# Kernel tuning notes

Hardware: AMD Instinct MI355X
Metric: run time of the kernel (lower is better)

The kernel has to match this reference:

```python
import jax, jax.numpy as jnp
import numpy as np

TOP_K = 2
LN_EPS = 1e-5
GATE_EPS = 1e-6


def setup_inputs() -> dict:
    key = jax.random.key(0)
    ks = jax.random.split(key, 5)
    B, D, E, H, O = 16384, 1200, 8, 1024, 1
    x = jax.random.normal(ks[0], (B, D), dtype=jnp.float32)
    w_gate = jax.random.normal(ks[1], (D, E), dtype=jnp.float32) * 0.05
    W1 = jax.random.normal(ks[2], (E, D, H), dtype=jnp.float32) * (1.0 / np.sqrt(D))
    b1 = jnp.zeros((E, H), dtype=jnp.float32)
    g1 = jnp.ones((E, H), dtype=jnp.float32)   # LayerNorm weight
    be1 = jnp.zeros((E, H), dtype=jnp.float32)  # LayerNorm bias
    W2 = jax.random.normal(ks[3], (E, H, O), dtype=jnp.float32) * (1.0 / np.sqrt(H))
    b2 = jnp.zeros((E, O), dtype=jnp.float32)
    return {"x": x, "w_gate": w_gate, "W1": W1, "b1": b1, "g1": g1, "be1": be1, "W2": W2, "b2": b2}


def reference(x, w_gate, W1, b1, g1, be1, W2, b2):
    B = x.shape[0]
    # --- top-k gating (eval mode: no noise) ---
    probs = jax.nn.softmax(x @ w_gate, axis=1)                 # [B, E]
    top_vals, top_idx = jax.lax.top_k(probs, TOP_K)            # [B, k]
    top_gates = top_vals / (jnp.sum(top_vals, axis=1, keepdims=True) + GATE_EPS)
    gates = jnp.zeros_like(probs).at[jnp.arange(B)[:, None], top_idx].set(top_gates)  # [B, E]
    # --- per-expert MLP (computed densely for all experts; gates zero out non-selected) ---
    h = jnp.einsum('bd,edh->beh', x, W1) + b1                  # [B, E, H]
    mu = jnp.mean(h, axis=-1, keepdims=True)
    var = jnp.var(h, axis=-1, keepdims=True)
    h = (h - mu) * jax.lax.rsqrt(var + LN_EPS) * g1 + be1      # LayerNorm
    h = jax.nn.relu(h)
    out = jax.nn.sigmoid(jnp.einsum('beh,eho->beo', h, W2) + b2)  # [B, E, O]
    # --- scatter/combine: weighted sum over experts ---
    y = jnp.einsum('be,beo->bo', gates, out)                   # [B, O]
    return y
```

## Files before the change

kernel.cpp:

```cpp
#include <hip/hip_runtime.h>
#include <hip/hip_bf16.h>
#include <stdint.h>

#define B_ROWS 16384
#define D_IN   1200
#define D_PAD  1216
#define N_EXP  8
#define H_DIM  1024
#define R_CAP  4608
#define CAP    36864
#define N_RT   288
#define LN_EPS 1e-5f
#define GATE_EPS 1e-6f
#define CNT_STRIDE 16

#define O_CNT    0
#define O_PROWC  512
#define O_PGATEC 147968
#define O_XBF    295424
#define O_W1T    40143744
#define O_HBUF   60066688

#define GATING_BLOCKS (B_ROWS / 16)
#define W1T_BLOCKS    (19 * 16 * 8)
#define PREP_BLOCKS   (GATING_BLOCKS + 1 + W1T_BLOCKS)

#define NT        (D_PAD / 32)
#define SLOT_SZ   16384

typedef short bf16x8 __attribute__((ext_vector_type(8)));
typedef short short8 __attribute__((ext_vector_type(8)));
typedef short short4v __attribute__((ext_vector_type(4)));
typedef float f32x4 __attribute__((ext_vector_type(4)));

__device__ __forceinline__ void load_lds16(const void* gptr, void* ldsptr) {
    __builtin_amdgcn_global_load_lds(
        (__attribute__((address_space(1))) void*)const_cast<void*>(gptr),
        (__attribute__((address_space(3))) void*)ldsptr, 16, 0, 0);
}

__device__ __forceinline__ short4v pack_bf16x4(float4 a) {
    union { short4v v; __hip_bfloat16 h[4]; } u;
    u.h[0] = __float2bfloat16(a.x); u.h[1] = __float2bfloat16(a.y);
    u.h[2] = __float2bfloat16(a.z); u.h[3] = __float2bfloat16(a.w);
    return u.v;
}

__global__ __launch_bounds__(256) void prep_kernel(
    const float* __restrict__ x, const float* __restrict__ wg,
    int* __restrict__ cnt, int* __restrict__ pairRowC, float* __restrict__ pairGateC,
    __hip_bfloat16* __restrict__ xbf, float* __restrict__ y,
    const float* __restrict__ W1, __hip_bfloat16* __restrict__ w1t)
{
    __shared__ int lcnt[N_EXP];
    __shared__ int base[N_EXP];
    __shared__ float tile[2][32][33];
    int bx = blockIdx.x;
    int tid = threadIdx.x;

    if (bx > GATING_BLOCKS) {
        int b = bx - GATING_BLOCKS - 1;
        int d0 = (b % 19) * 64;
        int h0 = ((b / 19) % 16) * 64;
        int e = b / (19 * 16);
        const float* src = W1 + (long)e * D_IN * H_DIM;

        int hs = tid & 15;
        int dr = tid >> 4;
#pragma unroll
        for (int s = 0; s < 4; ++s) {
            int dl = dr + 16 * s;
            int d = d0 + dl;
            float4 v = (d < D_IN)
                ? ((const float4*)(src + (long)d * H_DIM + h0))[hs]
                : (float4){0.f, 0.f, 0.f, 0.f};
            int drl = dl & 31;
            int hl = hs * 4;
            int Th = hl >> 5;
            int hh = hl & 31;
            tile[Th][drl][hh + 0] = v.x;
            tile[Th][drl][hh + 1] = v.y;
            tile[Th][drl][hh + 2] = v.z;
            tile[Th][drl][hh + 3] = v.w;
            if (s == 1) {
                __syncthreads();
                int T2 = tid >> 7, rr = tid & 127;
                int hl2 = rr >> 2, dseg = rr & 3;
                float f[8];
#pragma unroll
                for (int jj = 0; jj < 8; ++jj) f[jj] = tile[T2][dseg * 8 + jj][hl2];
                union { short8 v8; __hip_bfloat16 hh8[8]; } u;
#pragma unroll
                for (int jj = 0; jj < 8; ++jj) u.hh8[jj] = __float2bfloat16(f[jj]);
                int h = h0 + T2 * 32 + hl2;
                ((short8*)(w1t + (long)e * H_DIM * D_PAD + (long)h * D_PAD + d0))[dseg] = u.v8;
                __syncthreads();
            }
        }
        __syncthreads();
        {
            int T2 = tid >> 7, rr = tid & 127;
            int hl2 = rr >> 2, dseg = rr & 3;
            float f[8];
#pragma unroll
            for (int jj = 0; jj < 8; ++jj) f[jj] = tile[T2][dseg * 8 + jj][hl2];
            union { short8 v8; __hip_bfloat16 hh8[8]; } u;
#pragma unroll
            for (int jj = 0; jj < 8; ++jj) u.hh8[jj] = __float2bfloat16(f[jj]);
            int h = h0 + T2 * 32 + hl2;
            ((short8*)(w1t + (long)e * H_DIM * D_PAD + (long)h * D_PAD + d0 + 32))[dseg] = u.v8;
        }
        return;
    }

    if (bx == GATING_BLOCKS) {
        short8* xrow = (short8*)(xbf + (long)B_ROWS * D_PAD);
        if (tid < 152) xrow[tid] = (short8){0, 0, 0, 0, 0, 0, 0, 0};
        return;
    }

    if (tid < N_EXP) lcnt[tid] = 0;
    if (tid < 16) y[bx * 16 + tid] = 0.f;
    __syncthreads();

    int widx = tid >> 6;
    int lane = tid & 63;
    int rowbase = bx * 16 + widx * 4;
    const float* xw = x + (long)rowbase * D_IN;

    float acc[4][8];
#pragma unroll
    for (int r = 0; r < 4; ++r)
#pragma unroll
        for (int e = 0; e < N_EXP; ++e) acc[r][e] = 0.f;

    for (int i = lane; i < 304; i += 64) {
        if (i < 300) {
            const float4* wv4 = (const float4*)(wg + (long)i * 32);
            float4 w0 = wv4[0], w1v = wv4[1], w2 = wv4[2], w3 = wv4[3],
                   w4 = wv4[4], w5 = wv4[5], w6 = wv4[6], w7 = wv4[7];
#pragma unroll
            for (int r = 0; r < 4; ++r) {
                float4 xv = ((const float4*)(xw + (long)r * D_IN))[i];
                acc[r][0] += xv.x * w0.x + xv.y * w2.x + xv.z * w4.x + xv.w * w6.x;
                acc[r][1] += xv.x * w0.y + xv.y * w2.y + xv.z * w4.y + xv.w * w6.y;
                acc[r][2] += xv.x * w0.z + xv.y * w2.z + xv.z * w4.z + xv.w * w6.z;
                acc[r][3] += xv.x * w0.w + xv.y * w2.w + xv.z * w4.w + xv.w * w6.w;
                acc[r][4] += xv.x * w1v.x + xv.y * w3.x + xv.z * w5.x + xv.w * w7.x;
                acc[r][5] += xv.x * w1v.y + xv.y * w3.y + xv.z * w5.y + xv.w * w7.y;
                acc[r][6] += xv.x * w1v.z + xv.y * w3.z + xv.z * w5.z + xv.w * w7.z;
                acc[r][7] += xv.x * w1v.w + xv.y * w3.w + xv.z * w5.w + xv.w * w7.w;
                ((short4v*)(xbf + (long)(rowbase + r) * D_PAD))[i] = pack_bf16x4(xv);
            }
        } else {
#pragma unroll
            for (int r = 0; r < 4; ++r)
                ((short4v*)(xbf + (long)(rowbase + r) * D_PAD))[i] = (short4v){0, 0, 0, 0};
        }
    }

#pragma unroll
    for (int r = 0; r < 4; ++r)
#pragma unroll
        for (int e = 0; e < N_EXP; ++e) {
            float v = acc[r][e];
#pragma unroll
            for (int off = 32; off > 0; off >>= 1) v += __shfl_xor(v, off, 64);
            acc[r][e] = v;
        }

    float my[N_EXP];
#pragma unroll
    for (int e = 0; e < N_EXP; ++e) my[e] = acc[0][e];
#pragma unroll
    for (int r = 1; r < 4; ++r)
#pragma unroll
        for (int e = 0; e < N_EXP; ++e)
            if (lane == r) my[e] = acc[r][e];

    int i0 = 0, i1 = 1, s0 = 0, s1 = 0;
    float g0 = 0.f, g1 = 0.f;
    if (lane < 4) {
        float m = my[0];
#pragma unroll
        for (int e = 1; e < N_EXP; ++e) m = fmaxf(m, my[e]);
        float p[N_EXP], s = 0.f;
#pragma unroll
        for (int e = 0; e < N_EXP; ++e) { p[e] = expf(my[e] - m); s += p[e]; }
#pragma unroll
        for (int e = 1; e < N_EXP; ++e) if (p[e] > p[i0]) i0 = e;
        i1 = (i0 == 0) ? 1 : 0;
#pragma unroll
        for (int e = 0; e < N_EXP; ++e) if (e != i0 && p[e] > p[i1]) i1 = e;
        float v0 = p[i0] / s, v1 = p[i1] / s;
        float inv = 1.f / (v0 + v1 + GATE_EPS);
        g0 = v0 * inv; g1 = v1 * inv;
        s0 = atomicAdd(&lcnt[i0], 1);
        s1 = atomicAdd(&lcnt[i1], 1);
    }
    __syncthreads();
    if (tid < N_EXP) base[tid] = atomicAdd(&cnt[tid * CNT_STRIDE], lcnt[tid]);
    __syncthreads();
    if (lane < 4) {
        int row = rowbase + lane;
        int p0 = i0 * R_CAP + base[i0] + s0;
        pairRowC[p0] = row; pairGateC[p0] = g0;
        int p1 = i1 * R_CAP + base[i1] + s1;
        pairRowC[p1] = row; pairGateC[p1] = g1;
    }
}

__global__ __launch_bounds__(256) void gemm_kernel(
    const __hip_bfloat16* __restrict__ xbf, const __hip_bfloat16* __restrict__ w1t,
    const float* __restrict__ b1, const int* __restrict__ cnt,
    const int* __restrict__ pairRowC,
    __hip_bfloat16* __restrict__ hbuf)
{
    int bi = blockIdx.x;
    int xcd = bi & 7;
    int j = bi >> 3;
    int col0 = (j & 7) << 7;
    int rt = xcd * 36 + (j >> 3);
    int row0 = rt << 7;
    int e = xcd;
    int cnt_e = cnt[e * CNT_STRIDE];
    if (row0 - e * R_CAP >= cnt_e) return;

    __shared__ __attribute__((aligned(128))) char lds[3 * SLOT_SZ];

    int t = threadIdx.x;
    int lane = t & 63, w = t >> 6;
    int wm = (w >> 1) * 64, wn = (w & 1) * 64;
    int l15 = lane & 15, quad = lane >> 4;
    int qsw = quad ^ ((l15 >> 1) & 3);

    f32x4 acc[4][4];
#pragma unroll
    for (int i = 0; i < 4; ++i)
#pragma unroll
        for (int j2 = 0; j2 < 4; ++j2) acc[i][j2] = (f32x4){0.f, 0.f, 0.f, 0.f};

    int r1 = t >> 2, seg = t & 3;
    int sw = seg ^ ((r1 >> 1) & 3);
    int ridx1 = pairRowC[row0 + r1];
    int ridx2 = pairRowC[row0 + 64 + r1];
    ridx1 = ((unsigned)ridx1 > B_ROWS) ? B_ROWS : ridx1;
    ridx2 = ((unsigned)ridx2 > B_ROWS) ? B_ROWS : ridx2;
    const __hip_bfloat16* Arow1 = xbf + (long)ridx1 * D_PAD + sw * 8;
    const __hip_bfloat16* Arow2 = xbf + (long)ridx2 * D_PAD + sw * 8;
    const __hip_bfloat16* Bb = w1t + (long)e * H_DIM * D_PAD + (long)col0 * D_PAD;
    const __hip_bfloat16* Brow1 = Bb + (long)r1 * D_PAD + sw * 8;
    const __hip_bfloat16* Brow2 = Bb + (long)(r1 + 64) * D_PAD + sw * 8;

#define STAGE(sl, koff) do { \
    char* sb_ = lds + (sl) * SLOT_SZ; \
    load_lds16(Arow1 + (koff), sb_ + t * 16); \
    load_lds16(Arow2 + (koff), sb_ + 4096 + t * 16); \
    load_lds16(Brow1 + (koff), sb_ + 8192 + t * 16); \
    load_lds16(Brow2 + (koff), sb_ + 12288 + t * 16); } while (0)

    STAGE(0, 0);
    STAGE(1, 32);
    asm volatile("s_waitcnt vmcnt(4)" ::: "memory");
    __builtin_amdgcn_s_barrier();
    asm volatile("" ::: "memory");

    int cur = 0;
    for (int kt = 0; kt < NT; ++kt) {
        int nxt2 = cur + 2; if (nxt2 >= 3) nxt2 -= 3;
        if (kt + 2 < NT) STAGE(nxt2, (kt + 2) * 32);

        const char* lAc = lds + cur * SLOT_SZ;
        const char* lBc = lAc + 8192;
        bf16x8 af[4], bfr[4];
#pragma unroll
        for (int i = 0; i < 4; ++i)
            af[i] = *(const bf16x8*)(lAc + (wm + i * 16 + l15) * 64 + qsw * 16);
#pragma unroll
        for (int j2 = 0; j2 < 4; ++j2)
            bfr[j2] = *(const bf16x8*)(lBc + (wn + j2 * 16 + l15) * 64 + qsw * 16);
#pragma unroll
        for (int i = 0; i < 4; ++i)
#pragma unroll
            for (int j2 = 0; j2 < 4; ++j2)
                acc[i][j2] = __builtin_amdgcn_mfma_f32_16x16x32_bf16(af[i], bfr[j2], acc[i][j2], 0, 0, 0);

        if (kt + 2 < NT)      asm volatile("s_waitcnt vmcnt(4)" ::: "memory");
        else if (kt + 1 < NT) asm volatile("s_waitcnt vmcnt(0)" ::: "memory");
        if (kt + 1 < NT) {
            __builtin_amdgcn_s_barrier();
            asm volatile("" ::: "memory");
        }
        cur += 1; if (cur >= 3) cur -= 3;
    }
#undef STAGE

#pragma unroll
    for (int i = 0; i < 4; ++i) {
        int lr = wm + i * 16 + quad * 4;
#pragma unroll
        for (int j2 = 0; j2 < 4; ++j2) {
            int gc = col0 + wn + j2 * 16 + l15;
            float bias = b1[e * H_DIM + gc];
#pragma unroll
            for (int r = 0; r < 4; ++r) {
                float v = acc[i][j2][r] + bias;
                hbuf[(long)(row0 + lr + r) * H_DIM + gc] = __float2bfloat16(v);
            }
        }
    }
}

__global__ __launch_bounds__(256) void ln_head_kernel(
    const __hip_bfloat16* __restrict__ hbuf, const int* __restrict__ cnt,
    const int* __restrict__ pairRowC, const float* __restrict__ pairGateC,
    const float* __restrict__ g1, const float* __restrict__ be1,
    const float* __restrict__ W2, const float* __restrict__ b2,
    float* __restrict__ y)
{
    int tid = threadIdx.x;
    int p = blockIdx.x * 4 + (tid >> 6);
    int e = p / R_CAP;
    int slot = p - e * R_CAP;
    if (slot >= cnt[e * CNT_STRIDE]) return;

    int lane = tid & 63;
    int row = pairRowC[p];
    float gate = pairGateC[p];
    const short4v* hr = (const short4v*)(hbuf + (long)p * H_DIM);

    float v[16];
    float sum = 0.f, sumsq = 0.f;
#pragma unroll
    for (int k = 0; k < 4; ++k) {
        union { short4v s; __hip_bfloat16 h[4]; } hv;
        hv.s = hr[lane + k * 64];
#pragma unroll
        for (int j = 0; j < 4; ++j) {
            float f = __bfloat162float(hv.h[j]);
            v[k * 4 + j] = f;
            sum += f;
            sumsq += f * f;
        }
    }
#pragma unroll
    for (int off = 32; off > 0; off >>= 1) {
        sum += __shfl_xor(sum, off, 64);
        sumsq += __shfl_xor(sumsq, off, 64);
    }
    float mu = sum * (1.f / H_DIM);
    float var = sumsq * (1.f / H_DIM) - mu * mu;
    float rstd = rsqrtf(var + LN_EPS);

    float z = 0.f;
#pragma unroll
    for (int k = 0; k < 4; ++k) {
        float4 gv = ((const float4*)(g1 + e * H_DIM))[lane + k * 64];
        float4 bv = ((const float4*)(be1 + e * H_DIM))[lane + k * 64];
        float4 wv = ((const float4*)(W2 + e * H_DIM))[lane + k * 64];
        z += fmaxf((v[k*4+0] - mu) * rstd * gv.x + bv.x, 0.f) * wv.x;
        z += fmaxf((v[k*4+1] - mu) * rstd * gv.y + bv.y, 0.f) * wv.y;
        z += fmaxf((v[k*4+2] - mu) * rstd * gv.z + bv.z, 0.f) * wv.z;
        z += fmaxf((v[k*4+3] - mu) * rstd * gv.w + bv.w, 0.f) * wv.w;
    }
#pragma unroll
    for (int off = 32; off > 0; off >>= 1) z += __shfl_xor(z, off, 64);
    if (lane == 0) {
        float zt = z + b2[e];
        float o = 1.f / (1.f + expf(-zt));
        atomicAdd(&y[row], gate * o);
    }
}

extern "C" void kernel_launch(void* const* d_in, const int* in_sizes, int n_in,
                              void* d_out, int out_size, void* d_ws, size_t ws_size,
                              hipStream_t stream)
{
    const float* x   = (const float*)d_in[0];
    const float* wg  = (const float*)d_in[1];
    const float* W1  = (const float*)d_in[2];
    const float* b1  = (const float*)d_in[3];
    const float* g1  = (const float*)d_in[4];
    const float* be1 = (const float*)d_in[5];
    const float* W2  = (const float*)d_in[6];
    const float* b2  = (const float*)d_in[7];
    float* y = (float*)d_out;

    char* ws = (char*)d_ws;
    int*   cnt       = (int*)(ws + O_CNT);
    int*   pairRowC  = (int*)(ws + O_PROWC);
    float* pairGateC = (float*)(ws + O_PGATEC);
    __hip_bfloat16* xbf  = (__hip_bfloat16*)(ws + O_XBF);
    __hip_bfloat16* w1t  = (__hip_bfloat16*)(ws + O_W1T);
    __hip_bfloat16* hbuf = (__hip_bfloat16*)(ws + O_HBUF);

    hipMemsetAsync(cnt, 0, 512, stream);

    prep_kernel<<<PREP_BLOCKS, 256, 0, stream>>>(x, wg, cnt, pairRowC, pairGateC,
                                                 xbf, y, W1, w1t);
    gemm_kernel<<<N_RT * 8, 256, 0, stream>>>(xbf, w1t, b1, cnt, pairRowC, hbuf);
    ln_head_kernel<<<CAP / 4, 256, 0, stream>>>(hbuf, cnt, pairRowC, pairGateC,
                                                g1, be1, W2, b2, y);
}
```

Baseline: 307.4 us.

## Load A fragments directly from global and drop triple-buffered LDS pipeline

The expert GEMM no longer stages the gathered x rows through LDS. Each wave reads its A fragments straight from global memory via per-row pointers, and only the W1 tile goes into a single LDS buffer guarded by two __syncthreads per k-step. This removes the 3-slot async pipeline and cuts LDS footprint, which may help occupancy. The cost is that global loads are no longer overlapped with compute, A rows are fetched redundantly by the two column waves, and loads are exposed at every barrier.

```diff
diff --git a/kernel.cpp b/kernel.cpp
--- a/kernel.cpp
+++ b/kernel.cpp
@@ -26,7 +26,6 @@
 #define PREP_BLOCKS   (GATING_BLOCKS + 1 + W1T_BLOCKS)
 
 #define NT        (D_PAD / 32)
-#define SLOT_SZ   16384
 
 typedef short bf16x8 __attribute__((ext_vector_type(8)));
 typedef short short8 __attribute__((ext_vector_type(8)));
@@ -226,7 +225,7 @@
     int cnt_e = cnt[e * CNT_STRIDE];
     if (row0 - e * R_CAP >= cnt_e) return;
 
-    __shared__ __attribute__((aligned(128))) char lds[3 * SLOT_SZ];
+    __shared__ short lB[128 * 32];
 
     int t = threadIdx.x;
     int lane = t & 63, w = t >> 6;
@@ -240,42 +239,33 @@
 #pragma unroll
         for (int j2 = 0; j2 < 4; ++j2) acc[i][j2] = (f32x4){0.f, 0.f, 0.f, 0.f};
 
+    const __hip_bfloat16* Aptr[4];
+#pragma unroll
+    for (int i = 0; i < 4; ++i) {
+        int ridx = pairRowC[row0 + wm + i * 16 + l15];
+        ridx = ((unsigned)ridx > B_ROWS) ? B_ROWS : ridx;
+        Aptr[i] = xbf + (long)ridx * D_PAD + quad * 8;
+    }
+
     int r1 = t >> 2, seg = t & 3;
     int sw = seg ^ ((r1 >> 1) & 3);
-    int ridx1 = pairRowC[row0 + r1];
-    int ridx2 = pairRowC[row0 + 64 + r1];
-    ridx1 = ((unsigned)ridx1 > B_ROWS) ? B_ROWS : ridx1;
-    ridx2 = ((unsigned)ridx2 > B_ROWS) ? B_ROWS : ridx2;
-    const __hip_bfloat16* Arow1 = xbf + (long)ridx1 * D_PAD + sw * 8;
-    const __hip_bfloat16* Arow2 = xbf + (long)ridx2 * D_PAD + sw * 8;
     const __hip_bfloat16* Bb = w1t + (long)e * H_DIM * D_PAD + (long)col0 * D_PAD;
     const __hip_bfloat16* Brow1 = Bb + (long)r1 * D_PAD + sw * 8;
     const __hip_bfloat16* Brow2 = Bb + (long)(r1 + 64) * D_PAD + sw * 8;
-
-#define STAGE(sl, koff) do { \
-    char* sb_ = lds + (sl) * SLOT_SZ; \
-    load_lds16(Arow1 + (koff), sb_ + t * 16); \
-    load_lds16(Arow2 + (koff), sb_ + 4096 + t * 16); \
-    load_lds16(Brow1 + (koff), sb_ + 8192 + t * 16); \
-    load_lds16(Brow2 + (koff), sb_ + 12288 + t * 16); } while (0)
-
-    STAGE(0, 0);
-    STAGE(1, 32);
-    asm volatile("s_waitcnt vmcnt(4)" ::: "memory");
-    __builtin_amdgcn_s_barrier();
-    asm volatile("" ::: "memory");
-
-    int cur = 0;
+    char* lBc = (char*)lB;
+
     for (int kt = 0; kt < NT; ++kt) {
-        int nxt2 = cur + 2; if (nxt2 >= 3) nxt2 -= 3;
-        if (kt + 2 < NT) STAGE(nxt2, (kt + 2) * 32);
-
-        const char* lAc = lds + cur * SLOT_SZ;
-        const char* lBc = lAc + 8192;
-        bf16x8 af[4], bfr[4];
+        int k0 = kt * 32;
+        __syncthreads();
+        load_lds16(Brow1 + k0, lBc + t * 16);
+        load_lds16(Brow2 + k0, lBc + t * 16 + 4096);
+        bf16x8 af[4];
 #pragma unroll
         for (int i = 0; i < 4; ++i)
-            af[i] = *(const bf16x8*)(lAc + (wm + i * 16 + l15) * 64 + qsw * 16);
+            af[i] = *(const bf16x8*)(Aptr[i] + k0);
+        __syncthreads();
+
+        bf16x8 bfr[4];
 #pragma unroll
         for (int j2 = 0; j2 < 4; ++j2)
             bfr[j2] = *(const bf16x8*)(lBc + (wn + j2 * 16 + l15) * 64 + qsw * 16);
@@ -284,16 +274,7 @@
 #pragma unroll
             for (int j2 = 0; j2 < 4; ++j2)
                 acc[i][j2] = __builtin_amdgcn_mfma_f32_16x16x32_bf16(af[i], bfr[j2], acc[i][j2], 0, 0, 0);
-
-        if (kt + 2 < NT)      asm volatile("s_waitcnt vmcnt(4)" ::: "memory");
-        else if (kt + 1 < NT) asm volatile("s_waitcnt vmcnt(0)" ::: "memory");
-        if (kt + 1 < NT) {
-            __builtin_amdgcn_s_barrier();
-            asm volatile("" ::: "memory");
-        }
-        cur += 1; if (cur >= 3) cur -= 3;
-    }
-#undef STAGE
+    }
 
 #pragma unroll
     for (int i = 0; i < 4; ++i) {
```

After: 382.2 us. 1.24x slower.
